# Kernel optimization log

Hardware: AMD Instinct MI355X
Metric: run time of the kernel (lower is better)

The kernel has to match this reference:

```python
import jax, jax.numpy as jnp
import numpy as np

N_NODES = 50000
N_EDGES = 640000
D = 128  # node_dim == edge_dim (required by gate * Vh[dst])
BN_EPS = 1e-5


def _bn(x, gamma, beta):
    # BatchNorm1d in training mode: batch stats over dim 0, biased variance.
    mu = jnp.mean(x, axis=0)
    var = jnp.var(x, axis=0)
    return (x - mu) * jax.lax.rsqrt(var + BN_EPS) * gamma + beta


def setup_inputs() -> dict:
    key = jax.random.key(0)
    ks = jax.random.split(key, 12)
    s = 1.0 / np.sqrt(D)
    h = jax.random.normal(ks[0], (N_NODES, D), dtype=jnp.float32)
    e = jax.random.normal(ks[1], (N_EDGES, D), dtype=jnp.float32)
    edge_index = jax.random.randint(ks[2], (2, N_EDGES), 0, N_NODES)
    mk = lambda k: jax.random.uniform(k, (D, D), jnp.float32, -s, s)
    return {
        "h": h, "e": e, "edge_index": edge_index,
        "Pw": mk(ks[3]), "Qw": mk(ks[4]), "Rw": mk(ks[5]),
        "Uw": mk(ks[6]), "Vw": mk(ks[7]),
        "W1": mk(ks[8]), "b1": jnp.zeros((D,), jnp.float32),
        "W2": mk(ks[9]), "b2": jnp.zeros((D,), jnp.float32),
        "gamma_e": jnp.ones((D,), jnp.float32), "beta_e": jnp.zeros((D,), jnp.float32),
        "gamma_n": jnp.ones((D,), jnp.float32), "beta_n": jnp.zeros((D,), jnp.float32),
        "alpha": jnp.float32(1.0),
    }


def reference(h, e, edge_index, Pw, Qw, Rw, Uw, Vw, W1, b1, W2, b2,
              gamma_e, beta_e, gamma_n, beta_n, alpha):
    src, dst = edge_index[0], edge_index[1]
    # e_hat = P e + Q h[src] + R h[dst]   -> [E, D]
    e_hat = e @ Pw + h[src] @ Qw + h[dst] @ Rw
    # edge update: residual + MLP(BN(e_hat))
    z = _bn(e_hat, gamma_e, beta_e)
    e_new = e + jax.nn.relu(z @ W1 + b1) @ W2 + b2
    # node update: h + alpha * BN(U h + sum_j sigmoid(e_hat) * V h[dst])
    gate = jax.nn.sigmoid(e_hat)
    Vh = h @ Vw
    msg = gate * Vh[dst]                         # [E, D]
    agg = jax.ops.segment_sum(msg, src, num_segments=h.shape[0])
    h_new = h + alpha * _bn(h @ Uw + agg, gamma_n, beta_n)
    return (h_new, e_new)
```

## Files before the change

kernel.cpp:

```cpp
#include <hip/hip_runtime.h>


#define NN 50000
#define NE 640000
#define D 128

typedef unsigned int uint32;
typedef unsigned short u16;
typedef short bf16x8 __attribute__((ext_vector_type(8)));
typedef float floatx4 __attribute__((ext_vector_type(4)));

__device__ __forceinline__ u16 f2bf(float f) {
  uint32 u = __float_as_uint(f);
  u += 0x7fffu + ((u >> 16) & 1u);
  return (u16)(u >> 16);
}
__device__ __forceinline__ float bfu2f(uint32 lo16) { return __uint_as_float(lo16 << 16); }
__device__ __forceinline__ uint32 pack2(float a, float b) {
  return (uint32)f2bf(a) | ((uint32)f2bf(b) << 16);
}

__device__ __forceinline__ void mfma_tile64(const u16* __restrict__ Xs,
                                            const u16* __restrict__ Ws,
                                            floatx4 acc[8], int wave, int lane) {
  const int q = lane >> 4, l = lane & 15;
  const u16* ax = Xs + (wave * 16 + l) * 136 + q * 8;
  const u16* bx = Ws + l * 136 + q * 8;
#pragma unroll
  for (int kk = 0; kk < 4; ++kk) {
    bf16x8 a = *(const bf16x8*)(ax + kk * 32);
#pragma unroll
    for (int nt = 0; nt < 8; ++nt) {
      bf16x8 b = *(const bf16x8*)(bx + nt * 16 * 136 + kk * 32);
      acc[nt] = __builtin_amdgcn_mfma_f32_16x16x32_bf16(a, b, acc[nt], 0, 0, 0);
    }
  }
}

__global__ __launch_bounds__(256) void k_wconv(
    const float* __restrict__ Pw, const float* __restrict__ Qw, const float* __restrict__ Rw,
    const float* __restrict__ Uw, const float* __restrict__ Vw, const float* __restrict__ W1,
    const float* __restrict__ W2, u16* __restrict__ wt) {
  int b = blockIdx.x;
  const float* s = (b == 0) ? Pw : (b == 1) ? Qw : (b == 2) ? Rw : (b == 3) ? Uw
                 : (b == 4) ? Vw : (b == 5) ? W1 : W2;
  u16* dstp = wt + b * 16384;
  for (int idx = threadIdx.x; idx < 16384; idx += 256) {
    int k = idx >> 7, n = idx & 127;
    dstp[n * 128 + k] = f2bf(s[idx]);
  }
}

__global__ __launch_bounds__(256) void k_node_gemm(
    const float* __restrict__ h, const u16* __restrict__ wt, float* __restrict__ hQ,
    float* __restrict__ hR, float* __restrict__ hU, float* __restrict__ hV) {
  __shared__ u16 Xs[64 * 136];
  __shared__ u16 Ws[128 * 136];
  const int tid = threadIdx.x;
  const int wave = tid >> 6, lane = tid & 63;
  const int q = lane >> 4, l = lane & 15;
  const int row0 = blockIdx.x * 64;

#pragma unroll
  for (int it = 0; it < 8; ++it) {
    int idx = (it * 256 + tid) * 4;
    int r = idx >> 7, c = idx & 127;
    int g = row0 + r;
    float4 v = make_float4(0.f, 0.f, 0.f, 0.f);
    if (g < NN) v = *(const float4*)(h + (size_t)g * D + c);
    uint2 p;
    p.x = pack2(v.x, v.y);
    p.y = pack2(v.z, v.w);
    *(uint2*)(Xs + r * 136 + c) = p;
  }

  float* const outs[4] = {hQ, hR, hU, hV};
#pragma unroll
  for (int wi = 0; wi < 4; ++wi) {
#pragma unroll
    for (int it = 0; it < 8; ++it) {
      int idx = (it * 256 + tid) * 8;
      *(uint4*)(Ws + (idx >> 7) * 136 + (idx & 127)) =
          *(const uint4*)(wt + (wi + 1) * 16384 + idx);
    }
    __syncthreads();
    floatx4 acc[8] = {};
    mfma_tile64(Xs, Ws, acc, wave, lane);
    float* outp = outs[wi];
#pragma unroll
    for (int nt = 0; nt < 8; ++nt) {
#pragma unroll
      for (int r = 0; r < 4; ++r) {
        int m = wave * 16 + q * 4 + r;
        int g = row0 + m;
        if (g < NN) outp[(size_t)g * D + nt * 16 + l] = acc[nt][r];
      }
    }
    __syncthreads();
  }
}

__global__ __launch_bounds__(256) void k_edge1(
    const float* __restrict__ e, const int* __restrict__ src, const int* __restrict__ dst,
    const u16* __restrict__ wt, const float* __restrict__ hQ, const float* __restrict__ hR,
    const float* __restrict__ hV, u16* __restrict__ ehat, float* __restrict__ agg,
    float* __restrict__ esum, float* __restrict__ esq) {
  __shared__ u16 Xs[64 * 136];
  __shared__ u16 Ws[128 * 136];
  __shared__ int sSrc[64], sDst[64];
  __shared__ float sSum[128], sSq[128];
  const int tid = threadIdx.x;
  const int wave = tid >> 6, lane = tid & 63;
  const int q = lane >> 4, l = lane & 15;
  const int row0 = blockIdx.x * 64;

  if (tid < 128) { sSum[tid] = 0.f; sSq[tid] = 0.f; }
  if (tid < 64) { sSrc[tid] = src[row0 + tid]; sDst[tid] = dst[row0 + tid]; }
#pragma unroll
  for (int it = 0; it < 8; ++it) {
    int idx = (it * 256 + tid) * 4;
    int r = idx >> 7, c = idx & 127;
    float4 v = *(const float4*)(e + (size_t)(row0 + r) * D + c);
    uint2 p;
    p.x = pack2(v.x, v.y);
    p.y = pack2(v.z, v.w);
    *(uint2*)(Xs + r * 136 + c) = p;
  }
#pragma unroll
  for (int it = 0; it < 8; ++it) {
    int idx = (it * 256 + tid) * 8;
    *(uint4*)(Ws + (idx >> 7) * 136 + (idx & 127)) = *(const uint4*)(wt + idx);
  }
  __syncthreads();

  floatx4 acc[8] = {};
  mfma_tile64(Xs, Ws, acc, wave, lane);

  float cs[8] = {}, cq[8] = {};
#pragma unroll
  for (int nt = 0; nt < 8; ++nt) {
    const int n = nt * 16 + l;
#pragma unroll
    for (int r = 0; r < 4; ++r) {
      const int m = wave * 16 + q * 4 + r;
      const int s = sSrc[m], dd = sDst[m];
      float v = acc[nt][r] + hQ[(size_t)s * D + n] + hR[(size_t)dd * D + n];
      ehat[(size_t)(row0 + m) * D + n] = f2bf(v);
      float gate = 1.0f / (1.0f + __expf(-v));
      atomicAdd(&agg[(size_t)s * D + n], gate * hV[(size_t)dd * D + n]);
      cs[nt] += v;
      cq[nt] += v * v;
    }
  }
#pragma unroll
  for (int nt = 0; nt < 8; ++nt) {
    cs[nt] += __shfl_xor(cs[nt], 16);
    cs[nt] += __shfl_xor(cs[nt], 32);
    cq[nt] += __shfl_xor(cq[nt], 16);
    cq[nt] += __shfl_xor(cq[nt], 32);
    if (q == 0) {
      atomicAdd(&sSum[nt * 16 + l], cs[nt]);
      atomicAdd(&sSq[nt * 16 + l], cq[nt]);
    }
  }
  __syncthreads();
  if (tid < 128) {
    atomicAdd(&esum[(blockIdx.x & 31) * D + tid], sSum[tid]);
    atomicAdd(&esq[(blockIdx.x & 31) * D + tid], sSq[tid]);
  }
}

__global__ __launch_bounds__(256) void k_node_stats(const float* __restrict__ hU,
                                                    const float* __restrict__ agg,
                                                    float* __restrict__ nsum,
                                                    float* __restrict__ nsq) {
  __shared__ float4 Ls[256], Lq[256];
  const int tid = threadIdx.x;
  const int row0 = blockIdx.x * 64;
  const int c4 = (tid & 31) * 4, rs = tid >> 5;
  float4 s = make_float4(0.f, 0.f, 0.f, 0.f), sq = make_float4(0.f, 0.f, 0.f, 0.f);
#pragma unroll
  for (int i = 0; i < 8; ++i) {
    int g = row0 + i * 8 + rs;
    if (g < NN) {
      float4 u = *(const float4*)(hU + (size_t)g * D + c4);
      float4 a = *(const float4*)(agg + (size_t)g * D + c4);
      float x0 = u.x + a.x, x1 = u.y + a.y, x2 = u.z + a.z, x3 = u.w + a.w;
      s.x += x0; s.y += x1; s.z += x2; s.w += x3;
      sq.x += x0 * x0; sq.y += x1 * x1; sq.z += x2 * x2; sq.w += x3 * x3;
    }
  }
  Ls[tid] = s;
  Lq[tid] = sq;
  __syncthreads();
  if (tid < 128) {
    int grp = tid >> 2, comp = tid & 3;
    float ts = 0.f, tq = 0.f;
#pragma unroll
    for (int k = 0; k < 8; ++k) {
      ts += ((const float*)&Ls[k * 32 + grp])[comp];
      tq += ((const float*)&Lq[k * 32 + grp])[comp];
    }
    atomicAdd(&nsum[(blockIdx.x & 31) * D + tid], ts);
    atomicAdd(&nsq[(blockIdx.x & 31) * D + tid], tq);
  }
}

__global__ __launch_bounds__(128) void k_finalize(
    const float* __restrict__ esum, const float* __restrict__ esq,
    const float* __restrict__ nsum, const float* __restrict__ nsq,
    const float* __restrict__ ge, const float* __restrict__ be, const float* __restrict__ gn,
    const float* __restrict__ bnb, float* __restrict__ sce, float* __restrict__ she,
    float* __restrict__ scn, float* __restrict__ shn) {
  const int t = threadIdx.x;
  float s = 0.f, q = 0.f;
  for (int i = 0; i < 32; ++i) { s += esum[i * D + t]; q += esq[i * D + t]; }
  float mean = s / (float)NE;
  float var = q / (float)NE - mean * mean;
  float istd = rsqrtf(var + 1e-5f);
  sce[t] = istd * ge[t];
  she[t] = be[t] - mean * istd * ge[t];
  s = 0.f; q = 0.f;
  for (int i = 0; i < 32; ++i) { s += nsum[i * D + t]; q += nsq[i * D + t]; }
  mean = s / (float)NN;
  var = q / (float)NN - mean * mean;
  istd = rsqrtf(var + 1e-5f);
  scn[t] = istd * gn[t];
  shn[t] = bnb[t] - mean * istd * gn[t];
}

__global__ __launch_bounds__(256) void k_edge2(
    const u16* __restrict__ ehat, const float* __restrict__ e, const u16* __restrict__ wt,
    const float* __restrict__ sce, const float* __restrict__ she, const float* __restrict__ b1,
    const float* __restrict__ b2, float* __restrict__ oute) {
  __shared__ u16 Ts[64 * 136];
  __shared__ u16 Ws[128 * 136];
  __shared__ float sSc[128], sSh[128], sB1[128], sB2[128];
  const int tid = threadIdx.x;
  const int wave = tid >> 6, lane = tid & 63;
  const int q = lane >> 4, l = lane & 15;
  const int row0 = blockIdx.x * 64;

  if (tid < 128) { sSc[tid] = sce[tid]; sSh[tid] = she[tid]; sB1[tid] = b1[tid]; sB2[tid] = b2[tid]; }
  __syncthreads();

#pragma unroll
  for (int it = 0; it < 4; ++it) {
    int idx = (it * 256 + tid) * 8;
    int r = idx >> 7, c = idx & 127;
    uint4 u = *(const uint4*)(ehat + (size_t)(row0 + r) * D + c);
    float f0 = bfu2f(u.x & 0xffffu) * sSc[c + 0] + sSh[c + 0];
    float f1 = bfu2f(u.x >> 16) * sSc[c + 1] + sSh[c + 1];
    float f2 = bfu2f(u.y & 0xffffu) * sSc[c + 2] + sSh[c + 2];
    float f3 = bfu2f(u.y >> 16) * sSc[c + 3] + sSh[c + 3];
    float f4 = bfu2f(u.z & 0xffffu) * sSc[c + 4] + sSh[c + 4];
    float f5 = bfu2f(u.z >> 16) * sSc[c + 5] + sSh[c + 5];
    float f6 = bfu2f(u.w & 0xffffu) * sSc[c + 6] + sSh[c + 6];
    float f7 = bfu2f(u.w >> 16) * sSc[c + 7] + sSh[c + 7];
    uint4 o;
    o.x = pack2(f0, f1); o.y = pack2(f2, f3); o.z = pack2(f4, f5); o.w = pack2(f6, f7);
    *(uint4*)(Ts + r * 136 + c) = o;
  }
#pragma unroll
  for (int it = 0; it < 8; ++it) {
    int idx = (it * 256 + tid) * 8;
    *(uint4*)(Ws + (idx >> 7) * 136 + (idx & 127)) = *(const uint4*)(wt + 5 * 16384 + idx);
  }
  __syncthreads();

  floatx4 acc[8] = {};
  mfma_tile64(Ts, Ws, acc, wave, lane);
  __syncthreads();

#pragma unroll
  for (int nt = 0; nt < 8; ++nt) {
    int n = nt * 16 + l;
#pragma unroll
    for (int r = 0; r < 4; ++r) {
      int m = wave * 16 + q * 4 + r;
      float v = acc[nt][r] + sB1[n];
      Ts[m * 136 + n] = f2bf(fmaxf(v, 0.f));
    }
  }
#pragma unroll
  for (int it = 0; it < 8; ++it) {
    int idx = (it * 256 + tid) * 8;
    *(uint4*)(Ws + (idx >> 7) * 136 + (idx & 127)) = *(const uint4*)(wt + 6 * 16384 + idx);
  }
  __syncthreads();

  floatx4 acc2[8] = {};
  mfma_tile64(Ts, Ws, acc2, wave, lane);

#pragma unroll
  for (int nt = 0; nt < 8; ++nt) {
    int n = nt * 16 + l;
#pragma unroll
    for (int r = 0; r < 4; ++r) {
      int m = wave * 16 + q * 4 + r;
      size_t gi = (size_t)(row0 + m) * D + n;
      oute[gi] = e[gi] + acc2[nt][r] + sB2[n];
    }
  }
}

__global__ __launch_bounds__(256) void k_node_out(
    const float* __restrict__ h, const float* __restrict__ hU, const float* __restrict__ agg,
    const float* __restrict__ scn, const float* __restrict__ shn,
    const float* __restrict__ alphap, float* __restrict__ outh) {
  size_t idx = ((size_t)blockIdx.x * 256 + threadIdx.x) * 4;
  if (idx >= (size_t)NN * D) return;
  int c = (int)(idx & 127);
  float al = alphap[0];
  float4 u = *(const float4*)(hU + idx);
  float4 a = *(const float4*)(agg + idx);
  float4 hh = *(const float4*)(h + idx);
  float4 o;
  o.x = hh.x + al * ((u.x + a.x) * scn[c + 0] + shn[c + 0]);
  o.y = hh.y + al * ((u.y + a.y) * scn[c + 1] + shn[c + 1]);
  o.z = hh.z + al * ((u.z + a.z) * scn[c + 2] + shn[c + 2]);
  o.w = hh.w + al * ((u.w + a.w) * scn[c + 3] + shn[c + 3]);
  *(float4*)(outh + idx) = o;
}

extern "C" void kernel_launch(void* const* d_in, const int* in_sizes, int n_in, void* d_out,
                              int out_size, void* d_ws, size_t ws_size, hipStream_t stream) {
  const float* h = (const float*)d_in[0];
  const float* e = (const float*)d_in[1];
  const int* ei = (const int*)d_in[2];
  const float* Pw = (const float*)d_in[3];
  const float* Qw = (const float*)d_in[4];
  const float* Rw = (const float*)d_in[5];
  const float* Uw = (const float*)d_in[6];
  const float* Vw = (const float*)d_in[7];
  const float* W1 = (const float*)d_in[8];
  const float* b1 = (const float*)d_in[9];
  const float* W2 = (const float*)d_in[10];
  const float* b2 = (const float*)d_in[11];
  const float* ge = (const float*)d_in[12];
  const float* be = (const float*)d_in[13];
  const float* gn = (const float*)d_in[14];
  const float* bnb = (const float*)d_in[15];
  const float* al = (const float*)d_in[16];

  const int* srcp = ei;
  const int* dstp = ei + NE;

  char* ws = (char*)d_ws;
  u16* wt = (u16*)(ws);
  float* hQ = (float*)(ws + 229376ull);
  float* hR = (float*)(ws + 229376ull + 1ull * 25600000ull);
  float* hU = (float*)(ws + 229376ull + 2ull * 25600000ull);
  float* hV = (float*)(ws + 229376ull + 3ull * 25600000ull);
  float* agg = (float*)(ws + 229376ull + 4ull * 25600000ull);
  u16* ehat = (u16*)(ws + 229376ull + 5ull * 25600000ull);
  char* statb = ws + 229376ull + 5ull * 25600000ull + 163840000ull;
  float* esum = (float*)(statb);
  float* esq = (float*)(statb + 16384);
  float* nsum = (float*)(statb + 32768);
  float* nsq = (float*)(statb + 49152);
  float* sce = (float*)(statb + 65536);
  float* she = (float*)(statb + 65536 + 512);
  float* scn = (float*)(statb + 65536 + 1024);
  float* shn = (float*)(statb + 65536 + 1536);

  float* outh = (float*)d_out;
  float* oute = outh + (size_t)NN * D;

  hipMemsetAsync(agg, 0, (size_t)NN * D * sizeof(float), stream);
  hipMemsetAsync(statb, 0, 65536, stream);

  k_wconv<<<7, 256, 0, stream>>>(Pw, Qw, Rw, Uw, Vw, W1, W2, wt);
  k_node_gemm<<<782, 256, 0, stream>>>(h, wt, hQ, hR, hU, hV);
  k_edge1<<<10000, 256, 0, stream>>>(e, srcp, dstp, wt, hQ, hR, hV, ehat, agg, esum, esq);
  k_node_stats<<<782, 256, 0, stream>>>(hU, agg, nsum, nsq);
  k_finalize<<<1, 128, 0, stream>>>(esum, esq, nsum, nsq, ge, be, gn, bnb, sce, she, scn, shn);
  k_edge2<<<10000, 256, 0, stream>>>(ehat, e, wt, sce, she, b1, b2, oute);
  k_node_out<<<6250, 256, 0, stream>>>(h, hU, agg, scn, shn, al, outh);
}
```

Before: 1.120 ms.

## Replace atomic scatter aggregation with CSR-sorted gather and fused node stats

Builds a CSR grouping of edges by source node (histogram, single-block scan, atomic scatter) and replaces the per-element float atomicAdd into agg inside k_edge1 with a gather kernel. In that kernel one 32-lane group per node reads bf16 ehat and hV[dst], applies the sigmoid gate and accumulates in registers. The same kernel adds hU, writes the pre-BN node value and accumulates the node BN statistics, so the separate stats pass and the large agg memset go away. The trade-offs are three extra small kernels, a serial-ish single-block scan, a gate computed from bf16-rounded ehat, and uneven per-node degree loops.

```diff
diff --git a/kernel.cpp b/kernel.cpp
--- a/kernel.cpp
+++ b/kernel.cpp
@@ -100,11 +100,56 @@
   }
 }
 
+__global__ __launch_bounds__(256) void k_hist(const int* __restrict__ src,
+                                              int* __restrict__ cnt) {
+  int i = blockIdx.x * 256 + threadIdx.x;
+  if (i < NE) atomicAdd(&cnt[src[i]], 1);
+}
+
+__global__ __launch_bounds__(1024) void k_scan(const int* __restrict__ cnt,
+                                               int* __restrict__ offs) {
+  __shared__ int part[1024];
+  const int t = threadIdx.x;
+  const int base = t * 49;
+  int s = 0;
+  for (int j = 0; j < 49; ++j) {
+    int i = base + j;
+    if (i < NN) s += cnt[i];
+  }
+  part[t] = s;
+  __syncthreads();
+  for (int d = 1; d < 1024; d <<= 1) {
+    int v = (t >= d) ? part[t - d] : 0;
+    __syncthreads();
+    part[t] += v;
+    __syncthreads();
+  }
+  int run = (t == 0) ? 0 : part[t - 1];
+  for (int j = 0; j < 49; ++j) {
+    int i = base + j;
+    if (i < NN) {
+      offs[i] = run;
+      run += cnt[i];
+    }
+  }
+}
+
+__global__ __launch_bounds__(256) void k_scatter(const int* __restrict__ src,
+                                                 const int* __restrict__ dst,
+                                                 int* __restrict__ offs,
+                                                 int2* __restrict__ sorted) {
+  int i = blockIdx.x * 256 + threadIdx.x;
+  if (i < NE) {
+    int s = src[i];
+    int p = atomicAdd(&offs[s], 1);
+    sorted[p] = make_int2(i, dst[i]);
+  }
+}
+
 __global__ __launch_bounds__(256) void k_edge1(
     const float* __restrict__ e, const int* __restrict__ src, const int* __restrict__ dst,
     const u16* __restrict__ wt, const float* __restrict__ hQ, const float* __restrict__ hR,
-    const float* __restrict__ hV, u16* __restrict__ ehat, float* __restrict__ agg,
-    float* __restrict__ esum, float* __restrict__ esq) {
+    u16* __restrict__ ehat, float* __restrict__ esum, float* __restrict__ esq) {
   __shared__ u16 Xs[64 * 136];
   __shared__ u16 Ws[128 * 136];
   __shared__ int sSrc[64], sDst[64];
@@ -146,8 +191,6 @@
       const int s = sSrc[m], dd = sDst[m];
       float v = acc[nt][r] + hQ[(size_t)s * D + n] + hR[(size_t)dd * D + n];
       ehat[(size_t)(row0 + m) * D + n] = f2bf(v);
-      float gate = 1.0f / (1.0f + __expf(-v));
-      atomicAdd(&agg[(size_t)s * D + n], gate * hV[(size_t)dd * D + n]);
       cs[nt] += v;
       cq[nt] += v * v;
     }
@@ -170,39 +213,44 @@
   }
 }
 
-__global__ __launch_bounds__(256) void k_node_stats(const float* __restrict__ hU,
-                                                    const float* __restrict__ agg,
-                                                    float* __restrict__ nsum,
-                                                    float* __restrict__ nsq) {
-  __shared__ float4 Ls[256], Lq[256];
+__global__ __launch_bounds__(256) void k_agg(
+    const u16* __restrict__ ehat, const float* __restrict__ hV, const float* __restrict__ hU,
+    const int* __restrict__ cnt, const int* __restrict__ offs, const int2* __restrict__ sorted,
+    float* __restrict__ xb, float* __restrict__ nsum, float* __restrict__ nsq) {
+  __shared__ float sSum[128], sSq[128];
   const int tid = threadIdx.x;
-  const int row0 = blockIdx.x * 64;
-  const int c4 = (tid & 31) * 4, rs = tid >> 5;
-  float4 s = make_float4(0.f, 0.f, 0.f, 0.f), sq = make_float4(0.f, 0.f, 0.f, 0.f);
-#pragma unroll
-  for (int i = 0; i < 8; ++i) {
-    int g = row0 + i * 8 + rs;
-    if (g < NN) {
-      float4 u = *(const float4*)(hU + (size_t)g * D + c4);
-      float4 a = *(const float4*)(agg + (size_t)g * D + c4);
-      float x0 = u.x + a.x, x1 = u.y + a.y, x2 = u.z + a.z, x3 = u.w + a.w;
-      s.x += x0; s.y += x1; s.z += x2; s.w += x3;
-      sq.x += x0 * x0; sq.y += x1 * x1; sq.z += x2 * x2; sq.w += x3 * x3;
-    }
-  }
-  Ls[tid] = s;
-  Lq[tid] = sq;
+  if (tid < 128) { sSum[tid] = 0.f; sSq[tid] = 0.f; }
+  __syncthreads();
+  const int lane = tid & 31;
+  const int n = blockIdx.x * 8 + (tid >> 5);
+  const int end = offs[n];
+  const int deg = cnt[n];
+  const int p0 = end - deg;
+  float4 acc = make_float4(0.f, 0.f, 0.f, 0.f);
+  for (int k = 0; k < deg; ++k) {
+    int2 ed = sorted[p0 + k];
+    uint2 ev = *(const uint2*)(ehat + (size_t)ed.x * D + lane * 4);
+    float4 v = *(const float4*)(hV + (size_t)ed.y * D + lane * 4);
+    acc.x += v.x / (1.f + __expf(-bfu2f(ev.x & 0xffffu)));
+    acc.y += v.y / (1.f + __expf(-bfu2f(ev.x >> 16)));
+    acc.z += v.z / (1.f + __expf(-bfu2f(ev.y & 0xffffu)));
+    acc.w += v.w / (1.f + __expf(-bfu2f(ev.y >> 16)));
+  }
+  float4 u = *(const float4*)(hU + (size_t)n * D + lane * 4);
+  float4 x = make_float4(u.x + acc.x, u.y + acc.y, u.z + acc.z, u.w + acc.w);
+  *(float4*)(xb + (size_t)n * D + lane * 4) = x;
+  atomicAdd(&sSum[lane * 4 + 0], x.x);
+  atomicAdd(&sSum[lane * 4 + 1], x.y);
+  atomicAdd(&sSum[lane * 4 + 2], x.z);
+  atomicAdd(&sSum[lane * 4 + 3], x.w);
+  atomicAdd(&sSq[lane * 4 + 0], x.x * x.x);
+  atomicAdd(&sSq[lane * 4 + 1], x.y * x.y);
+  atomicAdd(&sSq[lane * 4 + 2], x.z * x.z);
+  atomicAdd(&sSq[lane * 4 + 3], x.w * x.w);
   __syncthreads();
   if (tid < 128) {
-    int grp = tid >> 2, comp = tid & 3;
-    float ts = 0.f, tq = 0.f;
-#pragma unroll
-    for (int k = 0; k < 8; ++k) {
-      ts += ((const float*)&Ls[k * 32 + grp])[comp];
-      tq += ((const float*)&Lq[k * 32 + grp])[comp];
-    }
-    atomicAdd(&nsum[(blockIdx.x & 31) * D + tid], ts);
-    atomicAdd(&nsq[(blockIdx.x & 31) * D + tid], tq);
+    atomicAdd(&nsum[(blockIdx.x & 31) * D + tid], sSum[tid]);
+    atomicAdd(&nsq[(blockIdx.x & 31) * D + tid], sSq[tid]);
   }
 }
 
@@ -305,21 +353,19 @@
 }
 
 __global__ __launch_bounds__(256) void k_node_out(
-    const float* __restrict__ h, const float* __restrict__ hU, const float* __restrict__ agg,
+    const float* __restrict__ h, const float* __restrict__ xb,
     const float* __restrict__ scn, const float* __restrict__ shn,
     const float* __restrict__ alphap, float* __restrict__ outh) {
   size_t idx = ((size_t)blockIdx.x * 256 + threadIdx.x) * 4;
-  if (idx >= (size_t)NN * D) return;
   int c = (int)(idx & 127);
   float al = alphap[0];
-  float4 u = *(const float4*)(hU + idx);
-  float4 a = *(const float4*)(agg + idx);
+  float4 x = *(const float4*)(xb + idx);
   float4 hh = *(const float4*)(h + idx);
   float4 o;
-  o.x = hh.x + al * ((u.x + a.x) * scn[c + 0] + shn[c + 0]);
-  o.y = hh.y + al * ((u.y + a.y) * scn[c + 1] + shn[c + 1]);
-  o.z = hh.z + al * ((u.z + a.z) * scn[c + 2] + shn[c + 2]);
-  o.w = hh.w + al * ((u.w + a.w) * scn[c + 3] + shn[c + 3]);
+  o.x = hh.x + al * (x.x * scn[c + 0] + shn[c + 0]);
+  o.y = hh.y + al * (x.y * scn[c + 1] + shn[c + 1]);
+  o.z = hh.z + al * (x.z * scn[c + 2] + shn[c + 2]);
+  o.w = hh.w + al * (x.w * scn[c + 3] + shn[c + 3]);
   *(float4*)(outh + idx) = o;
 }
 
@@ -352,7 +398,7 @@
   float* hR = (float*)(ws + 229376ull + 1ull * 25600000ull);
   float* hU = (float*)(ws + 229376ull + 2ull * 25600000ull);
   float* hV = (float*)(ws + 229376ull + 3ull * 25600000ull);
-  float* agg = (float*)(ws + 229376ull + 4ull * 25600000ull);
+  float* xb = (float*)(ws + 229376ull + 4ull * 25600000ull);
   u16* ehat = (u16*)(ws + 229376ull + 5ull * 25600000ull);
   char* statb = ws + 229376ull + 5ull * 25600000ull + 163840000ull;
   float* esum = (float*)(statb);
@@ -363,18 +409,25 @@
   float* she = (float*)(statb + 65536 + 512);
   float* scn = (float*)(statb + 65536 + 1024);
   float* shn = (float*)(statb + 65536 + 1536);
+  char* sortb = statb + 67584;
+  int* cnt = (int*)(sortb);
+  int* offs = (int*)(sortb + 200704);
+  int2* sorted = (int2*)(sortb + 401408);
 
   float* outh = (float*)d_out;
   float* oute = outh + (size_t)NN * D;
 
-  hipMemsetAsync(agg, 0, (size_t)NN * D * sizeof(float), stream);
+  hipMemsetAsync(cnt, 0, 200704, stream);
   hipMemsetAsync(statb, 0, 65536, stream);
 
   k_wconv<<<7, 256, 0, stream>>>(Pw, Qw, Rw, Uw, Vw, W1, W2, wt);
+  k_hist<<<2500, 256, 0, stream>>>(srcp, cnt);
+  k_scan<<<1, 1024, 0, stream>>>(cnt, offs);
+  k_scatter<<<2500, 256, 0, stream>>>(srcp, dstp, offs, sorted);
   k_node_gemm<<<782, 256, 0, stream>>>(h, wt, hQ, hR, hU, hV);
-  k_edge1<<<10000, 256, 0, stream>>>(e, srcp, dstp, wt, hQ, hR, hV, ehat, agg, esum, esq);
-  k_node_stats<<<782, 256, 0, stream>>>(hU, agg, nsum, nsq);
+  k_edge1<<<10000, 256, 0, stream>>>(e, srcp, dstp, wt, hQ, hR, ehat, esum, esq);
+  k_agg<<<6250, 256, 0, stream>>>(ehat, hV, hU, cnt, offs, sorted, xb, nsum, nsq);
   k_finalize<<<1, 128, 0, stream>>>(esum, esq, nsum, nsq, ge, be, gn, bnb, sce, she, scn, shn);
   k_edge2<<<10000, 256, 0, stream>>>(ehat, e, wt, sce, she, b1, b2, oute);
-  k_node_out<<<6250, 256, 0, stream>>>(h, hU, agg, scn, shn, al, outh);
-}
+  k_node_out<<<6250, 256, 0, stream>>>(h, xb, scn, shn, al, outh);
+}
```

Result: slower. 1.204 ms (+7.5%).
